# Kernel optimization log

Measured on AMD Instinct MI355X. Metric: run time of the kernel, lower is better.

## Reference

```python
import jax, jax.numpy as jnp
import numpy as np

V, E, H, B, S, T, OOV = 50000, 128, 256, 32, 400, 16, 20


def setup_inputs() -> dict:
    key = jax.random.key(0)
    ks = jax.random.split(key, 20)
    def p(i, shape, s=0.02):
        return jax.random.normal(ks[i], shape, dtype=jnp.float32) * s
    z = lambda *shape: jnp.zeros(shape, dtype=jnp.float32)
    return {
        'input_seq': jax.random.randint(ks[0], (B, S), 0, V),
        'input_seq_ext': jax.random.randint(ks[1], (B, S), 0, V + OOV),
        'target_seq': jax.random.randint(ks[2], (B, T), 0, V),
        'embedding': p(3, (V, E)),
        'enc_Wih_f': p(4, (3 * H, E)), 'enc_Whh_f': p(5, (3 * H, H)),
        'enc_bih_f': z(3 * H), 'enc_bhh_f': z(3 * H),
        'enc_Wih_b': p(6, (3 * H, E)), 'enc_Whh_b': p(7, (3 * H, H)),
        'enc_bih_b': z(3 * H), 'enc_bhh_b': z(3 * H),
        'proj_W': p(8, (H, 2 * H)), 'proj_b': z(H),
        'bridge_W': p(9, (H, 2 * H)), 'bridge_b': z(H),
        'dec_Wih': p(10, (3 * H, E + 2 * H)), 'dec_Whh': p(11, (3 * H, H)),
        'dec_bih': z(3 * H), 'dec_bhh': z(3 * H),
        'attn_Wq': p(12, (H, H)), 'attn_We': p(13, (1, H)),
        'lin_W': p(14, (H, E + 3 * H)), 'lin_b': z(H),
        'pgen_W': p(15, (1, E + 3 * H)), 'pgen_b': z(1),
        'out_W': p(16, (V, H)), 'out_b': z(V),
    }


def gru_cell(x, h, Wih, Whh, bih, bhh):
    # PyTorch GRU cell math
    gi = x @ Wih.T + bih
    gh = h @ Whh.T + bhh
    ir, iz, inn = jnp.split(gi, 3, axis=-1)
    hr, hz, hn = jnp.split(gh, 3, axis=-1)
    r = jax.nn.sigmoid(ir + hr)
    zg = jax.nn.sigmoid(iz + hz)
    n = jnp.tanh(inn + r * hn)
    return (1.0 - zg) * n + zg * h


def run_gru(xs, h0, Wih, Whh, bih, bhh):
    def step(h, x):
        h2 = gru_cell(x, h, Wih, Whh, bih, bhh)
        return h2, h2
    hT, hs = jax.lax.scan(step, h0, xs)
    return hs, hT


def reference(input_seq, input_seq_ext, target_seq, embedding,
              enc_Wih_f, enc_Whh_f, enc_bih_f, enc_bhh_f,
              enc_Wih_b, enc_Whh_b, enc_bih_b, enc_bhh_b,
              proj_W, proj_b, bridge_W, bridge_b,
              dec_Wih, dec_Whh, dec_bih, dec_bhh,
              attn_Wq, attn_We, lin_W, lin_b,
              pgen_W, pgen_b, out_W, out_b):
    Bsz, Slen = input_seq.shape
    Tlen = target_seq.shape[1]
    Hd = bridge_W.shape[0]
    dt = embedding.dtype

    # ---- encoder (bidirectional GRU) ----
    emb_src = embedding[input_seq].transpose(1, 0, 2)  # (S,B,E)
    h0e = jnp.zeros((Bsz, Hd), dt)
    hs_f, hf = run_gru(emb_src, h0e, enc_Wih_f, enc_Whh_f, enc_bih_f, enc_bhh_f)
    hs_b_rev, hb = run_gru(emb_src[::-1], h0e, enc_Wih_b, enc_Whh_b, enc_bih_b, enc_bhh_b)
    enc_states = jnp.concatenate([hs_f, hs_b_rev[::-1]], axis=-1)  # (S,B,2H)
    proj = enc_states @ proj_W.T + proj_b                           # (S,B,H)
    h = jnp.tanh(jnp.concatenate([hf, hb], axis=-1) @ bridge_W.T + bridge_b)  # (B,H)

    rows = jnp.arange(Bsz)
    toks = target_seq[:, :Tlen - 1].T  # teacher forcing, (T-1,B)

    def dec_step(h, tok):
        e = embedding[tok]                                            # (B,E)
        scores = jnp.tanh(h @ attn_Wq.T + proj) @ attn_We[0]          # (S,B)
        alphas = jax.nn.softmax(scores, axis=0)                       # softmax over seq dim
        context = jnp.einsum('sb,sbd->bd', alphas, enc_states)        # (B,2H)
        h2 = gru_cell(jnp.concatenate([e, context], axis=-1), h,
                      dec_Wih, dec_Whh, dec_bih, dec_bhh)             # (B,H)
        cat = jnp.concatenate([e, h2, context], axis=-1)              # (B,E+3H)
        p_gen = jax.nn.sigmoid(cat @ pgen_W.T + pgen_b)               # (B,1)
        logits = (cat @ lin_W.T + lin_b) @ out_W.T + out_b            # (B,V)
        gen = p_gen * jax.nn.softmax(logits, axis=-1)
        attn = (1.0 - p_gen) * alphas.T                               # (B,S)
        ext = jnp.concatenate([gen, jnp.zeros((Bsz, OOV), dt)], axis=-1) + 1e-12
        ext = ext.at[rows[:, None], input_seq_ext].add(attn)          # scatter_add copy dist
        return h2, jnp.log(ext)

    _, outs = jax.lax.scan(dec_step, h, toks)                         # (T-1,B,V+OOV)
    out0 = jnp.zeros((1,) + outs.shape[1:], outs.dtype)               # t=0 row stays zero
    return jnp.concatenate([out0, outs], axis=0)                      # (T,B,V+OOV)
```

## Files before the change

kernel.cpp:

```cpp
#include <hip/hip_runtime.h>

#define SLEN 400
#define BATCH 32
#define TLEN 16
#define NDEC 15
#define EDIM 128
#define HDIM 256
#define H3 768
#define VVOC 50000
#define VEXT 50020
#define SCHUNK 50

__device__ __forceinline__ float frcp(float x){ return __builtin_amdgcn_rcpf(x); }
__device__ __forceinline__ float fsig(float x){ return frcp(1.f + __expf(-x)); }
__device__ __forceinline__ float ftanh(float x){
  float e = __expf(2.f*x);
  return 1.f - 2.f*frcp(e + 1.f);
}

typedef _Float16 h2 __attribute__((ext_vector_type(2)));
typedef _Float16 half8 __attribute__((ext_vector_type(8)));
typedef float floatx4 __attribute__((ext_vector_type(4)));

__device__ __forceinline__ h2 u2h(unsigned u){ return __builtin_bit_cast(h2, u); }
__device__ __forceinline__ unsigned pkh(float a, float b){
  h2 v; v.x=(_Float16)a; v.y=(_Float16)b;
  return __builtin_bit_cast(unsigned, v);
}

#if __has_builtin(__builtin_amdgcn_fdot2)
__device__ __forceinline__ float fdot2h(h2 a, h2 b, float c){
  return __builtin_amdgcn_fdot2(a, b, c, false);
}
#else
__device__ __forceinline__ float fdot2h(h2 a, h2 b, float c){
  return fmaf((float)a.x,(float)b.x, fmaf((float)a.y,(float)b.y, c));
}
#endif

#if __has_builtin(__builtin_amdgcn_sdot4)
__device__ __forceinline__ int sdot4(unsigned a, unsigned b, int c){
  return __builtin_amdgcn_sdot4((int)a, (int)b, c, false);
}
#else
__device__ __forceinline__ int sdot4(unsigned a, unsigned b, int c){
  #pragma unroll
  for (int k=0;k<4;++k)
    c += (int)(char)((a>>(8*k))&0xFF) * (int)(char)((b>>(8*k))&0xFF);
  return c;
}
#endif

__device__ __forceinline__ float wred_sum(float v){
  #pragma unroll
  for (int o=32;o>0;o>>=1) v += __shfl_down(v,o,64);
  return v;
}
__device__ __forceinline__ float wred_max(float v){
  #pragma unroll
  for (int o=32;o>0;o>>=1) v = fmaxf(v, __shfl_down(v,o,64));
  return v;
}
__device__ __forceinline__ float block_sum(float v, float* red){
  v = wred_sum(v);
  int lane = threadIdx.x & 63, wid = threadIdx.x >> 6;
  if (!lane) red[wid] = v;
  __syncthreads();
  if (threadIdx.x == 0){
    float m = red[0];
    int nw = blockDim.x >> 6;
    for (int w=1;w<nw;++w) m += red[w];
    red[0] = m;
  }
  __syncthreads();
  v = red[0];
  __syncthreads();
  return v;
}

__global__ __launch_bounds__(64) void k_embed(
    const int* __restrict__ input_seq, const int* __restrict__ target_seq,
    const float* __restrict__ embedding,
    _Float16* __restrict__ emb16, float* __restrict__ cat_all, _Float16* __restrict__ cat16)
{
  int row = blockIdx.x;
  if (row < SLEN*BATCH) {
    int s = row >> 5, b = row & 31;
    int tok = input_seq[b*SLEN + s];
    float2 v = ((const float2*)(embedding + (size_t)tok*EDIM))[threadIdx.x];
    ((unsigned*)(emb16 + (size_t)row*EDIM))[threadIdx.x] = pkh(v.x, v.y);
  } else {
    int rr = row - SLEN*BATCH;
    int t = rr >> 5, b = rr & 31;
    int tok = target_seq[b*TLEN + t];
    float2 v = ((const float2*)(embedding + (size_t)tok*EDIM))[threadIdx.x];
    ((float2*)(cat_all + (size_t)rr*896))[threadIdx.x] = v;
    ((unsigned*)(cat16 + (size_t)rr*896))[threadIdx.x] = pkh(v.x, v.y);
  }
}

__global__ __launch_bounds__(256) void k_cvtv5(
    const float* __restrict__ S0, _Float16* __restrict__ D0, int n0,
    const float* __restrict__ S1, _Float16* __restrict__ D1, int n1,
    const float* __restrict__ S2, _Float16* __restrict__ D2, int n2,
    const float* __restrict__ S3, _Float16* __restrict__ D3, int n3,
    const float* __restrict__ S4, _Float16* __restrict__ D4, int n4)
{
  const float* S; _Float16* D; int n8;
  switch (blockIdx.y){
    case 0: S=S0; D=D0; n8=n0; break;
    case 1: S=S1; D=D1; n8=n1; break;
    case 2: S=S2; D=D2; n8=n2; break;
    case 3: S=S3; D=D3; n8=n3; break;
    default: S=S4; D=D4; n8=n4; break;
  }
  int i = blockIdx.x*256 + threadIdx.x;
  if (i >= n8) return;
  float4 a = ((const float4*)S)[i*2];
  float4 b = ((const float4*)S)[i*2+1];
  uint4 o;
  o.x = pkh(a.x,a.y); o.y = pkh(a.z,a.w);
  o.z = pkh(b.x,b.y); o.w = pkh(b.z,b.w);
  ((uint4*)D)[i] = o;
}

__global__ __launch_bounds__(256) void k_cvtv(
    const float* __restrict__ S, _Float16* __restrict__ D, int n8)
{
  int i = blockIdx.x*256 + threadIdx.x;
  if (i >= n8) return;
  float4 a = ((const float4*)S)[i*2];
  float4 b = ((const float4*)S)[i*2+1];
  uint4 o;
  o.x = pkh(a.x,a.y); o.y = pkh(a.z,a.w);
  o.z = pkh(b.x,b.y); o.w = pkh(b.z,b.w);
  ((uint4*)D)[i] = o;
}

__global__ __launch_bounds__(64) void k_cvtk3(
    const float* __restrict__ W0, uint4* __restrict__ D0,
    const float* __restrict__ W1, uint4* __restrict__ D1,
    const float* __restrict__ W2, uint4* __restrict__ D2)
{
  const float* W; uint4* D; int ldw, coloff, nrows, nk8;
  switch (blockIdx.y){
    case 0: W=W0; D=D0; ldw=640;  coloff=128; nrows=H3;   nk8=64; break;
    case 1: W=W1; D=D1; ldw=HDIM; coloff=0;   nrows=H3;   nk8=32; break;
    default: W=W2; D=D2; ldw=HDIM; coloff=0;  nrows=HDIM; nk8=32; break;
  }
  int row = blockIdx.x, k8 = threadIdx.x;
  if (row >= nrows || k8 >= nk8) return;
  const float* s = W + (size_t)row*ldw + coloff + k8*8;
  float4 x = *(const float4*)s;
  float4 y = *(const float4*)(s+4);
  uint4 o;
  o.x = pkh(x.x,x.y); o.y = pkh(x.z,x.w);
  o.z = pkh(y.x,y.y); o.w = pkh(y.z,y.w);
  D[(size_t)k8*nrows + row] = o;
}

__global__ __launch_bounds__(64) void k_cvti8(
    const float* __restrict__ Wf, uint4* __restrict__ Df,
    const float* __restrict__ Wb, uint4* __restrict__ Db,
    float* __restrict__ scl)
{
  int row = blockIdx.x, dir = blockIdx.y;
  const float* W = dir ? Wb : Wf;
  uint4* D = dir ? Db : Df;
  int t = threadIdx.x;
  const float* src = W + (size_t)row*HDIM;
  float m = 0.f;
  #pragma unroll
  for (int k=0;k<4;++k) m = fmaxf(m, fabsf(src[t*4+k]));
  m = wred_max(m);
  m = __shfl(m, 0, 64);
  float inv = (m > 0.f) ? 127.f/m : 0.f;
  if (t == 0) scl[dir*H3 + row] = (m > 0.f) ? m/(127.f*127.f) : 0.f;
  if (t < 16){
    unsigned u[4];
    #pragma unroll
    for (int q=0;q<4;++q){
      unsigned uu = 0;
      #pragma unroll
      for (int k=0;k<4;++k){
        int iv = (int)rintf(src[t*16 + q*4 + k]*inv);
        iv = iv > 127 ? 127 : (iv < -127 ? -127 : iv);
        uu |= ((unsigned)(iv & 0xFF)) << (8*k);
      }
      u[q] = uu;
    }
    uint4 o; o.x=u[0]; o.y=u[1]; o.z=u[2]; o.w=u[3];
    D[(size_t)t*H3 + row] = o;
  }
}

__global__ __launch_bounds__(256) void k_gmm(
    const _Float16* __restrict__ A, int lda,
    const _Float16* __restrict__ W, int ldw,
    const float* __restrict__ bias,
    float* __restrict__ C, _Float16* __restrict__ C16, int ldc,
    int M, int N, int K, int rev)
{
  __shared__ __align__(16) _Float16 Al[128*64];
  __shared__ __align__(16) _Float16 Wl[128*64];
  int tid = threadIdx.x;
  int wv = tid >> 6, l = tid & 63;
  int wr = (wv>>1)*64, wc = (wv&1)*64;
  int lr = l & 15, lh = l >> 4;
  int m0 = blockIdx.y*128, n0 = blockIdx.x*128;
  floatx4 acc[4][4];
  #pragma unroll
  for (int i=0;i<4;++i)
    #pragma unroll
    for (int jn=0;jn<4;++jn) acc[i][jn] = (floatx4){0.f,0.f,0.f,0.f};

  for (int kc=0; kc<K; kc+=64){
    #pragma unroll
    for (int i=0;i<4;++i){
      int idx = tid + i*256;
      int row = idx>>3, c = idx&7;
      int m = m0+row;
      uint4 v = {0u,0u,0u,0u};
      if (m < M){
        int am = m;
        if (rev){ int s = m>>5; am = ((SLEN-1-s)<<5)|(m&31); }
        v = *(const uint4*)&A[(size_t)am*lda + kc + c*8];
      }
      *(uint4*)&Al[row*64 + ((c ^ (row&7))<<3)] = v;
    }
    #pragma unroll
    for (int i=0;i<4;++i){
      int idx = tid + i*256;
      int row = idx>>3, c = idx&7;
      int n = n0+row;
      uint4 v = {0u,0u,0u,0u};
      if (n < N) v = *(const uint4*)&W[(size_t)n*ldw + kc + c*8];
      *(uint4*)&Wl[row*64 + ((c ^ (row&7))<<3)] = v;
    }
    __syncthreads();
    #pragma unroll
    for (int ks=0; ks<2; ++ks){
      half8 af0, af1, af2, af3, bf0, bf1, bf2, bf3;
      {
        int c = ks*4 + lh;
        int r0 = wr + 0*16 + lr, r1 = wr + 1*16 + lr, r2 = wr + 2*16 + lr, r3 = wr + 3*16 + lr;
        af0 = *(const half8*)&Al[r0*64 + ((c ^ (r0&7))<<3)];
        af1 = *(const half8*)&Al[r1*64 + ((c ^ (r1&7))<<3)];
        af2 = *(const half8*)&Al[r2*64 + ((c ^ (r2&7))<<3)];
        af3 = *(const half8*)&Al[r3*64 + ((c ^ (r3&7))<<3)];
        int n0l = wc + 0*16 + lr, n1l = wc + 1*16 + lr, n2l = wc + 2*16 + lr, n3l = wc + 3*16 + lr;
        bf0 = *(const half8*)&Wl[n0l*64 + ((c ^ (n0l&7))<<3)];
        bf1 = *(const half8*)&Wl[n1l*64 + ((c ^ (n1l&7))<<3)];
        bf2 = *(const half8*)&Wl[n2l*64 + ((c ^ (n2l&7))<<3)];
        bf3 = *(const half8*)&Wl[n3l*64 + ((c ^ (n3l&7))<<3)];
      }
      half8 afs[4] = {af0, af1, af2, af3};
      half8 bfs[4] = {bf0, bf1, bf2, bf3};
      #pragma unroll
      for (int mi=0;mi<4;++mi)
        #pragma unroll
        for (int ni=0;ni<4;++ni)
          acc[mi][ni] = __builtin_amdgcn_mfma_f32_16x16x32_f16(afs[mi], bfs[ni], acc[mi][ni], 0,0,0);
    }
    __syncthreads();
  }
  #pragma unroll
  for (int mi=0;mi<4;++mi){
    #pragma unroll
    for (int q=0;q<4;++q){
      int m = m0 + wr + mi*16 + lh*4 + q;
      if (m < M){
        #pragma unroll
        for (int ni=0;ni<4;++ni){
          int n = n0 + wc + ni*16 + lr;
          if (n < N){
            float v = acc[mi][ni][q] + bias[n];
            if (C)   C[(size_t)m*ldc + n] = v;
            if (C16) C16[(size_t)m*ldc + n] = (_Float16)v;
          }
        }
      }
    }
  }
}

__global__ __launch_bounds__(768) void k_enc(
    const _Float16* __restrict__ gi16_f, const _Float16* __restrict__ gi16_b,
    const uint4* __restrict__ Wi8_f, const uint4* __restrict__ Wi8_b,
    const float* __restrict__ scl_i8,
    const float* __restrict__ bhh_f, const float* __restrict__ bhh_b,
    _Float16* __restrict__ enc16, float* __restrict__ hfin)
{
  int dir = blockIdx.x >> 5, b = blockIdx.x & 31;
  int jj = threadIdx.x;
  const _Float16* gi = dir ? gi16_b : gi16_f;
  const uint4* Wi8p = (dir ? Wi8_b : Wi8_f) + jj;
  float scl = scl_i8[dir*H3 + jj];
  float bh = (dir ? bhh_b : bhh_f)[jj];

  __shared__ __align__(16) unsigned h8u[HDIM/4];
  __shared__ __align__(16) float st[H3];
  __shared__ uint4 Wlds[9][H3];

  #pragma unroll
  for (int p=0;p<9;++p) Wlds[p][jj] = Wi8p[p*H3];

  if (jj < HDIM/4) h8u[jj] = 0u;
  float hreg = 0.f;
  _Float16* dst = enc16 + (size_t)b*2*HDIM + dir*HDIM + jj;
  __syncthreads();

  for (int s=0;s<SLEN;++s){
    const _Float16* grow = gi + ((size_t)s*BATCH + b)*H3;
    float g1 = 0.f, g2 = 0.f;
    if (jj < 512)  g1 = (float)grow[jj];
    if (jj < HDIM) g2 = (float)grow[2*HDIM + jj];
    int is0=0, is1=0, is2=0, is3=0;
    #pragma unroll
    for (int p=0;p<9;++p){
      uint4 w = Wlds[p][jj];
      uint4 hq = *(const uint4*)&h8u[4*p];
      is0 = sdot4(w.x, hq.x, is0);
      is1 = sdot4(w.y, hq.y, is1);
      is2 = sdot4(w.z, hq.z, is2);
      is3 = sdot4(w.w, hq.w, is3);
    }
    #pragma unroll
    for (int p=9;p<16;++p){
      uint4 w = Wi8p[(size_t)p*H3];
      uint4 hq = *(const uint4*)&h8u[4*p];
      is0 = sdot4(w.x, hq.x, is0);
      is1 = sdot4(w.y, hq.y, is1);
      is2 = sdot4(w.z, hq.z, is2);
      is3 = sdot4(w.w, hq.w, is3);
    }
    float acc = (float)((is0+is1)+(is2+is3))*scl + bh;
    st[jj] = (jj < 512) ? (acc + g1) : acc;
    __syncthreads();
    if (jj < HDIM){
      float rr = fsig(st[jj]);
      float zz = fsig(st[HDIM + jj]);
      float nn = ftanh(g2 + rr*st[2*HDIM + jj]);
      float h2v = nn + zz*(hreg - nn);
      hreg = h2v;
      int srow = dir ? (SLEN-1-s) : s;
      dst[(size_t)srow*BATCH*2*HDIM] = (_Float16)h2v;
      int iv = (int)rintf(h2v*127.f);
      iv = iv > 127 ? 127 : (iv < -127 ? -127 : iv);
      ((char*)h8u)[jj] = (char)iv;
      if (s == SLEN-1) hfin[(size_t)(dir*BATCH + b)*HDIM + jj] = h2v;
    }
    __syncthreads();
  }
}

__global__ __launch_bounds__(256) void k_bridge(
    const float* __restrict__ hfin,
    const float* __restrict__ bridge_W, const float* __restrict__ bridge_b,
    float* __restrict__ h_out)
{
  int b = blockIdx.x, j = threadIdx.x;
  __shared__ float hcat[2*HDIM];
  hcat[j]        = hfin[(size_t)b*HDIM + j];
  hcat[HDIM + j] = hfin[(size_t)(BATCH + b)*HDIM + j];
  __syncthreads();
  const float* w = bridge_W + (size_t)j*2*HDIM;
  float4 a = {0.f,0.f,0.f,0.f};
  #pragma unroll 4
  for (int k=0;k<2*HDIM;k+=4){
    float4 h4 = *(const float4*)&hcat[k];
    float4 w4 = *(const float4*)&w[k];
    a.x=fmaf(h4.x,w4.x,a.x); a.y=fmaf(h4.y,w4.y,a.y);
    a.z=fmaf(h4.z,w4.z,a.z); a.w=fmaf(h4.w,w4.w,a.w);
  }
  h_out[b*HDIM+j] = ftanh((a.x+a.y)+(a.z+a.w) + bridge_b[j]);
}

__global__ __launch_bounds__(256) void k_attnB(
    int t,
    const _Float16* __restrict__ proj16,
    const _Float16* __restrict__ enc16,
    const uint4* __restrict__ Wq16k,
    const float* __restrict__ attn_We,
    const float* __restrict__ hin,
    float* __restrict__ alphas_e,
    float* __restrict__ sum_part,
    float* __restrict__ ctx_part)
{
  int ch = blockIdx.x, b = blockIdx.y;
  int tid = threadIdx.x;
  __shared__ float q_s[HDIM], we_s[HDIM], sc[SCHUNK], red[8];
  __shared__ __align__(16) unsigned hq[HDIM/2];

  we_s[tid] = attn_We[tid];
  if (tid < HDIM/2){
    float2 hv = *(const float2*)&hin[b*HDIM + tid*2];
    hq[tid] = pkh(hv.x, hv.y);
  }
  __syncthreads();
  {
    float a0=0.f,a1=0.f,a2=0.f,a3=0.f;
    #pragma unroll
    for (int k8=0;k8<32;++k8){
      uint4 w = Wq16k[(size_t)k8*HDIM + tid];
      uint4 hp = *(const uint4*)&hq[k8*4];
      a0 = fdot2h(u2h(w.x),u2h(hp.x),a0);
      a1 = fdot2h(u2h(w.y),u2h(hp.y),a1);
      a2 = fdot2h(u2h(w.z),u2h(hp.z),a2);
      a3 = fdot2h(u2h(w.w),u2h(hp.w),a3);
    }
    q_s[tid] = (a0+a1)+(a2+a3);
  }
  __syncthreads();
  {
    int wave = tid >> 6, lane = tid & 63;
    int d0 = lane*4;
    float4 qv = *(const float4*)&q_s[d0];
    float4 wv = *(const float4*)&we_s[d0];
    for (int is = wave; is < SCHUNK; is += 4){
      int s = ch*SCHUNK + is;
      uint2 p = *(const uint2*)&proj16[((size_t)(s*BATCH + b))*HDIM + d0];
      h2 pa = u2h(p.x), pb = u2h(p.y);
      float v = ftanh(qv.x+(float)pa.x)*wv.x + ftanh(qv.y+(float)pa.y)*wv.y
              + ftanh(qv.z+(float)pb.x)*wv.z + ftanh(qv.w+(float)pb.y)*wv.w;
      v = wred_sum(v);
      if (lane == 0){
        float e = __expf(v);
        sc[is] = e;
        alphas_e[((size_t)t*SLEN + s)*BATCH + b] = e;
      }
    }
  }
  __syncthreads();
  {
    float sv = (tid < SCHUNK) ? sc[tid] : 0.f;
    sv = block_sum(sv, red);
    if (tid == 0) sum_part[b*8 + ch] = sv;
  }
  {
    float a0=0.f, a1=0.f;
    for (int is=0; is<SCHUNK; ++is){
      int s = ch*SCHUNK + is;
      unsigned u = *(const unsigned*)&enc16[((size_t)(s*BATCH + b) << 9) + tid*2];
      h2 ev = u2h(u);
      float e = sc[is];
      a0 = fmaf(e, (float)ev.x, a0);
      a1 = fmaf(e, (float)ev.y, a1);
    }
    float2 o; o.x = a0; o.y = a1;
    *(float2*)&ctx_part[(((size_t)b*8 + ch) << 9) + tid*2] = o;
  }
}

__global__ __launch_bounds__(256) void k_gruD(
    int t,
    const float* __restrict__ ctx_part,
    const float* __restrict__ sum_part,
    const float* __restrict__ gie_all,
    const uint4* __restrict__ dWck16,
    const uint4* __restrict__ dWhk16,
    const float* __restrict__ dec_bhh,
    const float* __restrict__ hin,
    float* __restrict__ hout,
    float* __restrict__ cat_all, _Float16* __restrict__ cat16,
    float* __restrict__ sums_all)
{
  int ch = blockIdx.x, b = blockIdx.y;
  int tid = threadIdx.x;
  int jl = tid & 31, slice = tid >> 5;
  __shared__ __align__(16) unsigned cpk[HDIM], hpk[HDIM/2];
  __shared__ float hf[HDIM];
  __shared__ float pc[3][8][32], ph[3][8][32];
  __shared__ float invs;

  if (tid == 0){
    float ssum = 0.f;
    #pragma unroll
    for (int c=0;c<8;++c) ssum += sum_part[b*8 + c];
    float inv = 1.f/ssum;
    invs = inv;
    if (ch == 0) sums_all[t*BATCH + b] = inv;
  }
  if (tid < HDIM/2){
    float2 hv = *(const float2*)&hin[b*HDIM + tid*2];
    hpk[tid] = pkh(hv.x, hv.y);
    hf[tid*2] = hv.x; hf[tid*2+1] = hv.y;
  }
  __syncthreads();
  {
    int d0 = tid*2;
    float c0=0.f, c1=0.f;
    #pragma unroll
    for (int c=0;c<8;++c){
      float2 v = *(const float2*)&ctx_part[(((size_t)b*8 + c) << 9) + d0];
      c0 += v.x; c1 += v.y;
    }
    c0 *= invs; c1 *= invs;
    cpk[tid] = pkh(c0, c1);
    if (ch == 0){
      int r = t*BATCH + b;
      cat_all[(size_t)r*896 + 384 + d0]     = c0;
      cat_all[(size_t)r*896 + 384 + d0 + 1] = c1;
      cat16[(size_t)r*896 + 384 + d0]     = (_Float16)c0;
      cat16[(size_t)r*896 + 384 + d0 + 1] = (_Float16)c1;
    }
  }
  __syncthreads();
  {
    int jb = ch*32 + jl;
    float c0=0.f,c1=0.f,c2=0.f, g0=0.f,g1=0.f,g2=0.f;
    #pragma unroll
    for (int i=0;i<8;++i){
      int k8 = slice*8 + i;
      uint4 hq = *(const uint4*)&cpk[k8*4];
      uint4 w0 = dWck16[(size_t)k8*H3 + jb];
      uint4 w1 = dWck16[(size_t)k8*H3 + 256 + jb];
      uint4 w2 = dWck16[(size_t)k8*H3 + 512 + jb];
      c0 = fdot2h(u2h(w0.x),u2h(hq.x),c0); c0 = fdot2h(u2h(w0.y),u2h(hq.y),c0);
      c0 = fdot2h(u2h(w0.z),u2h(hq.z),c0); c0 = fdot2h(u2h(w0.w),u2h(hq.w),c0);
      c1 = fdot2h(u2h(w1.x),u2h(hq.x),c1); c1 = fdot2h(u2h(w1.y),u2h(hq.y),c1);
      c1 = fdot2h(u2h(w1.z),u2h(hq.z),c1); c1 = fdot2h(u2h(w1.w),u2h(hq.w),c1);
      c2 = fdot2h(u2h(w2.x),u2h(hq.x),c2); c2 = fdot2h(u2h(w2.y),u2h(hq.y),c2);
      c2 = fdot2h(u2h(w2.z),u2h(hq.z),c2); c2 = fdot2h(u2h(w2.w),u2h(hq.w),c2);
    }
    #pragma unroll
    for (int i=0;i<4;++i){
      int k8 = slice*4 + i;
      uint4 hq = *(const uint4*)&hpk[k8*4];
      uint4 w0 = dWhk16[(size_t)k8*H3 + jb];
      uint4 w1 = dWhk16[(size_t)k8*H3 + 256 + jb];
      uint4 w2 = dWhk16[(size_t)k8*H3 + 512 + jb];
      g0 = fdot2h(u2h(w0.x),u2h(hq.x),g0); g0 = fdot2h(u2h(w0.y),u2h(hq.y),g0);
      g0 = fdot2h(u2h(w0.z),u2h(hq.z),g0); g0 = fdot2h(u2h(w0.w),u2h(hq.w),g0);
      g1 = fdot2h(u2h(w1.x),u2h(hq.x),g1); g1 = fdot2h(u2h(w1.y),u2h(hq.y),g1);
      g1 = fdot2h(u2h(w1.z),u2h(hq.z),g1); g1 = fdot2h(u2h(w1.w),u2h(hq.w),g1);
      g2 = fdot2h(u2h(w2.x),u2h(hq.x),g2); g2 = fdot2h(u2h(w2.y),u2h(hq.y),g2);
      g2 = fdot2h(u2h(w2.z),u2h(hq.z),g2); g2 = fdot2h(u2h(w2.w),u2h(hq.w),g2);
    }
    pc[0][slice][jl]=c0; pc[1][slice][jl]=c1; pc[2][slice][jl]=c2;
    ph[0][slice][jl]=g0; ph[1][slice][jl]=g1; ph[2][slice][jl]=g2;
  }
  __syncthreads();
  if (tid < 32){
    int j = tid, r = t*BATCH + b;
    int jj = ch*32 + j;
    float gi0 = gie_all[(size_t)r*H3 + jj];
    float gi1 = gie_all[(size_t)r*H3 + 256 + jj];
    float gi2 = gie_all[(size_t)r*H3 + 512 + jj];
    float gh0 = dec_bhh[jj], gh1 = dec_bhh[256 + jj], gh2 = dec_bhh[512 + jj];
    #pragma unroll
    for (int c=0;c<8;++c){
      gi0 += pc[0][c][j]; gi1 += pc[1][c][j]; gi2 += pc[2][c][j];
      gh0 += ph[0][c][j]; gh1 += ph[1][c][j]; gh2 += ph[2][c][j];
    }
    float rr = fsig(gi0 + gh0);
    float zz = fsig(gi1 + gh1);
    float nn = ftanh(gi2 + rr*gh2);
    float hp = hf[jj];
    float h2v = nn + zz*(hp - nn);
    hout[b*HDIM + jj] = h2v;
    cat_all[(size_t)r*896 + 128 + jj] = h2v;
    cat16[(size_t)r*896 + 128 + jj] = (_Float16)h2v;
  }
}

__global__ __launch_bounds__(64) void k_pgen(
    const float* __restrict__ cat_all,
    const float* __restrict__ pgen_W, const float* __restrict__ pgen_b,
    float* __restrict__ pgen_all)
{
  int r = blockIdx.x;
  const float* c = cat_all + (size_t)r*896;
  float acc = 0.f;
  for (int k=threadIdx.x; k<896; k+=64) acc = fmaf(c[k], pgen_W[k], acc);
  acc = wred_sum(acc);
  if (threadIdx.x==0) pgen_all[r] = fsig(acc + pgen_b[0]);
}

__global__ __launch_bounds__(256) void k_rowsum(
    const _Float16* __restrict__ logits, float* __restrict__ row_sum)
{
  int r = blockIdx.x;
  const uint4* row = (const uint4*)(logits + (size_t)r*VVOC);
  __shared__ float red[8];
  float s = 0.f;
  for (int v=threadIdx.x; v<VVOC/8; v+=256){
    uint4 x = row[v];
    h2 a=u2h(x.x), bb=u2h(x.y), c=u2h(x.z), d=u2h(x.w);
    s += __expf((float)a.x) + __expf((float)a.y) + __expf((float)bb.x) + __expf((float)bb.y)
       + __expf((float)c.x) + __expf((float)c.y) + __expf((float)d.x) + __expf((float)d.y);
  }
  s = block_sum(s, red);
  if (threadIdx.x==0) row_sum[r] = 1.f/s;
}

__global__ __launch_bounds__(512) void k_scatter(
    const int* __restrict__ input_seq_ext,
    const float* __restrict__ alphas_e, const float* __restrict__ sums_all,
    const float* __restrict__ pgen_all,
    float* __restrict__ out)
{
  int r = blockIdx.x;
  int s = threadIdx.x;
  if (s >= SLEN) return;
  int t = r >> 5, b = r & 31;
  float w = (1.f - pgen_all[r]) * alphas_e[((size_t)t*SLEN + s)*BATCH + b] * sums_all[r];
  int idx = input_seq_ext[b*SLEN + s];
  atomicAdd(&out[((size_t)(t+1)*BATCH + b)*VEXT + idx], w);
}

__global__ __launch_bounds__(256) void k_final2(
    const _Float16* __restrict__ logits, const float* __restrict__ pgen_all,
    const float* __restrict__ row_sum,
    float* __restrict__ out)
{
  int v = blockIdx.x*256 + threadIdx.x;
  if (v >= VEXT) return;
  int b = blockIdx.y, t = blockIdx.z + 1;
  size_t o = ((size_t)t*BATCH + b)*VEXT + v;
  int r = (t-1)*BATCH + b;
  float val = out[o] + 1e-12f;
  if (v < VVOC)
    val += pgen_all[r] * row_sum[r] * __expf((float)logits[(size_t)r*VVOC + v]);
  out[o] = __logf(val);
}

extern "C" void kernel_launch(void* const* d_in, const int* in_sizes, int n_in,
                              void* d_out, int out_size, void* d_ws, size_t ws_size,
                              hipStream_t stream)
{
  (void)in_sizes; (void)n_in; (void)ws_size;
  const int*   input_seq     = (const int*)d_in[0];
  const int*   input_seq_ext = (const int*)d_in[1];
  const int*   target_seq    = (const int*)d_in[2];
  const float* embedding     = (const float*)d_in[3];
  const float* enc_Wih_f     = (const float*)d_in[4];
  const float* enc_Whh_f     = (const float*)d_in[5];
  const float* enc_bih_f     = (const float*)d_in[6];
  const float* enc_bhh_f     = (const float*)d_in[7];
  const float* enc_Wih_b     = (const float*)d_in[8];
  const float* enc_Whh_b     = (const float*)d_in[9];
  const float* enc_bih_b     = (const float*)d_in[10];
  const float* enc_bhh_b     = (const float*)d_in[11];
  const float* proj_W        = (const float*)d_in[12];
  const float* proj_b        = (const float*)d_in[13];
  const float* bridge_W      = (const float*)d_in[14];
  const float* bridge_b      = (const float*)d_in[15];
  const float* dec_Wih       = (const float*)d_in[16];
  const float* dec_Whh       = (const float*)d_in[17];
  const float* dec_bih       = (const float*)d_in[18];
  const float* dec_bhh       = (const float*)d_in[19];
  const float* attn_Wq       = (const float*)d_in[20];
  const float* attn_We       = (const float*)d_in[21];
  const float* lin_W         = (const float*)d_in[22];
  const float* lin_b         = (const float*)d_in[23];
  const float* pgen_W        = (const float*)d_in[24];
  const float* pgen_b        = (const float*)d_in[25];
  const float* out_W         = (const float*)d_in[26];
  const float* out_b         = (const float*)d_in[27];
  float* out = (float*)d_out;
  float* ws  = (float*)d_ws;

  _Float16* emb16    = (_Float16*)(ws + 0);
  _Float16* Wih16_f  = (_Float16*)(ws + 409600);
  _Float16* Wih16_b  = (_Float16*)(ws + 458752);
  _Float16* proj_W16 = (_Float16*)(ws + 507904);
  _Float16* lin_W16  = (_Float16*)(ws + 573440);
  _Float16* cat16    = (_Float16*)(ws + 688128);
  _Float16* lin16    = (_Float16*)(ws + 903168);
  _Float16* dWih16   = (_Float16*)(ws + 964608);
  _Float16* enc16    = (_Float16*)(ws + 1638400);
  float* hfin        = ws + 4915200;
  _Float16* proj16   = (_Float16*)(ws + 8192000);
  _Float16* gi16_f   = (_Float16*)(ws + 11468800);
  _Float16* gi16_b   = (_Float16*)(ws + 16384000);
  _Float16* logits16 = (_Float16*)(ws + 11468800);
  _Float16* out_W16  = (_Float16*)(ws + 23468800);
  uint4* Wq16k       = (uint4*)(ws + 33145600);
  uint4* dWck16      = (uint4*)(ws + 33178368);
  uint4* dWhk16      = (uint4*)(ws + 33374976);
  float* ctx_part    = ws + 33473280;
  float* sum_part    = ws + 33604352;
  float* sums_all    = ws + 33604608;
  float* hbuf0       = ws + 33605088;
  float* hbuf1       = ws + 33613280;
  uint4* Wi8_f       = (uint4*)(ws + 33621472);
  uint4* Wi8_b       = (uint4*)(ws + 33670624);
  float* scl_i8      = ws + 33719776;
  float* cat_all     = ws + 35468800;
  float* gie_all     = ws + 35898880;
  float* alphas_e    = ws + 36275712;
  float* pgen_all    = ws + 36467712;
  float* row_sum     = ws + 36468192;

  (void)hipMemsetAsync(out, 0, (size_t)out_size*sizeof(float), stream);

  k_embed<<<dim3(SLEN*BATCH + NDEC*BATCH), dim3(64), 0, stream>>>(
      input_seq, target_seq, embedding, emb16, cat_all, cat16);

  k_cvtv5<<<dim3(240, 5), dim3(256), 0, stream>>>(
      enc_Wih_f, Wih16_f, 12288,
      enc_Wih_b, Wih16_b, 12288,
      proj_W,    proj_W16, 16384,
      lin_W,     lin_W16,  28672,
      dec_Wih,   dWih16,   61440);
  k_cvtk3<<<dim3(H3, 3), dim3(64), 0, stream>>>(
      dec_Wih,   dWck16,
      dec_Whh,   dWhk16,
      attn_Wq,   Wq16k);
  k_cvti8<<<dim3(H3, 2), dim3(64), 0, stream>>>(enc_Whh_f, Wi8_f, enc_Whh_b, Wi8_b, scl_i8);

  k_gmm<<<dim3(6,100), dim3(256), 0, stream>>>(emb16, EDIM, Wih16_f, EDIM, enc_bih_f,
      (float*)nullptr, gi16_f, H3, SLEN*BATCH, H3, EDIM, 0);
  k_gmm<<<dim3(6,100), dim3(256), 0, stream>>>(emb16, EDIM, Wih16_b, EDIM, enc_bih_b,
      (float*)nullptr, gi16_b, H3, SLEN*BATCH, H3, EDIM, 1);

  k_enc<<<dim3(64), dim3(768), 0, stream>>>(gi16_f, gi16_b, Wi8_f, Wi8_b,
      scl_i8, enc_bhh_f, enc_bhh_b, enc16, hfin);

  k_cvtv<<<dim3((12800000/8+255)/256), dim3(256), 0, stream>>>(out_W, out_W16, 12800000/8);

  k_gmm<<<dim3(2,100), dim3(256), 0, stream>>>(enc16, 2*HDIM, proj_W16, 2*HDIM, proj_b,
      (float*)nullptr, proj16, HDIM, SLEN*BATCH, HDIM, 2*HDIM, 0);

  k_bridge<<<dim3(BATCH), dim3(256), 0, stream>>>(hfin, bridge_W, bridge_b, hbuf0);

  k_gmm<<<dim3(6,4), dim3(256), 0, stream>>>(cat16, 896, dWih16, 640, dec_bih,
      gie_all, (_Float16*)nullptr, H3, NDEC*BATCH, H3, EDIM, 0);

  float* hb[2] = {hbuf0, hbuf1};
  for (int t=0;t<NDEC;++t){
    k_attnB<<<dim3(8,32), dim3(256), 0, stream>>>(t, proj16, enc16, Wq16k, attn_We,
        hb[t&1], alphas_e, sum_part, ctx_part);
    k_gruD<<<dim3(8,32), dim3(256), 0, stream>>>(t, ctx_part, sum_part, gie_all,
        dWck16, dWhk16, dec_bhh, hb[t&1], hb[(t+1)&1], cat_all, cat16, sums_all);
  }

  k_gmm<<<dim3(2,4), dim3(256), 0, stream>>>(cat16, 896, lin_W16, 896, lin_b,
      (float*)nullptr, lin16, HDIM, NDEC*BATCH, HDIM, 896, 0);
  k_pgen<<<dim3(NDEC*BATCH), dim3(64), 0, stream>>>(cat_all, pgen_W, pgen_b, pgen_all);
  k_gmm<<<dim3(391,4), dim3(256), 0, stream>>>(lin16, HDIM, out_W16, HDIM, out_b,
      (float*)nullptr, logits16, VVOC, NDEC*BATCH, VVOC, HDIM, 0);
  k_rowsum<<<dim3(NDEC*BATCH), dim3(256), 0, stream>>>(logits16, row_sum);
  k_scatter<<<dim3(NDEC*BATCH), dim3(512), 0, stream>>>(input_seq_ext, alphas_e, sums_all, pgen_all, out);
  k_final2<<<dim3(196, BATCH, NDEC), dim3(256), 0, stream>>>(logits16, pgen_all, row_sum, out);
}
```

Measured before the change: 1.022 ms.

## Fuse out_W conversion into encoder, softmax rowsum into GEMM, query proj into GRU

The out_W fp32-to-fp16 conversion now runs in 200 extra blocks of the encoder recurrence kernel, so it overlaps with the latency-bound serial encoder instead of being a separate launch. The softmax exp-sum moves into the vocab GEMM epilogue through shuffle reduction and atomics, which removes the k_rowsum pass over the logits. The attention query projection is computed as per-chunk partials in the decoder GRU kernel (and in the bridge for the first step), so k_attnB only sums those partials. The encoder LDS weight cache also drops from 9 to 8 slices. The costs are atomic contention, exp sums taken from fp32 values rather than fp16-rounded ones, and possible slowdown of the encoder from the co-resident conversion blocks.

After: 1.136 ms. 1.11x slower.

```diff
diff --git a/kernel.cpp b/kernel.cpp
--- a/kernel.cpp
+++ b/kernel.cpp
@@ -124,19 +124,6 @@
   ((uint4*)D)[i] = o;
 }
 
-__global__ __launch_bounds__(256) void k_cvtv(
-    const float* __restrict__ S, _Float16* __restrict__ D, int n8)
-{
-  int i = blockIdx.x*256 + threadIdx.x;
-  if (i >= n8) return;
-  float4 a = ((const float4*)S)[i*2];
-  float4 b = ((const float4*)S)[i*2+1];
-  uint4 o;
-  o.x = pkh(a.x,a.y); o.y = pkh(a.z,a.w);
-  o.z = pkh(b.x,b.y); o.w = pkh(b.z,b.w);
-  ((uint4*)D)[i] = o;
-}
-
 __global__ __launch_bounds__(64) void k_cvtk3(
     const float* __restrict__ W0, uint4* __restrict__ D0,
     const float* __restrict__ W1, uint4* __restrict__ D1,
@@ -199,7 +186,7 @@
     const _Float16* __restrict__ W, int ldw,
     const float* __restrict__ bias,
     float* __restrict__ C, _Float16* __restrict__ C16, int ldc,
-    int M, int N, int K, int rev)
+    int M, int N, int K, int rev, float* __restrict__ expsum)
 {
   __shared__ __align__(16) _Float16 Al[128*64];
   __shared__ __align__(16) _Float16 Wl[128*64];
@@ -269,6 +256,7 @@
     #pragma unroll
     for (int q=0;q<4;++q){
       int m = m0 + wr + mi*16 + lh*4 + q;
+      float psum = 0.f;
       if (m < M){
         #pragma unroll
         for (int ni=0;ni<4;++ni){
@@ -277,8 +265,14 @@
             float v = acc[mi][ni][q] + bias[n];
             if (C)   C[(size_t)m*ldc + n] = v;
             if (C16) C16[(size_t)m*ldc + n] = (_Float16)v;
+            if (expsum) psum += __expf(v);
           }
         }
+      }
+      if (expsum){
+        #pragma unroll
+        for (int o=8;o>0;o>>=1) psum += __shfl_down(psum, o, 16);
+        if (lr == 0 && m < M) atomicAdd(&expsum[m], psum);
       }
     }
   }
@@ -289,8 +283,22 @@
     const uint4* __restrict__ Wi8_f, const uint4* __restrict__ Wi8_b,
     const float* __restrict__ scl_i8,
     const float* __restrict__ bhh_f, const float* __restrict__ bhh_b,
-    _Float16* __restrict__ enc16, float* __restrict__ hfin)
-{
+    _Float16* __restrict__ enc16, float* __restrict__ hfin,
+    const float* __restrict__ outW, _Float16* __restrict__ outW16)
+{
+  if (blockIdx.x >= 64){
+    int idx = (int)(blockIdx.x - 64)*768 + (int)threadIdx.x;
+    const int stride = 200*768;
+    for (int i = idx; i < 1600000; i += stride){
+      float4 a = ((const float4*)outW)[i*2];
+      float4 b2 = ((const float4*)outW)[i*2+1];
+      uint4 o;
+      o.x = pkh(a.x,a.y); o.y = pkh(a.z,a.w);
+      o.z = pkh(b2.x,b2.y); o.w = pkh(b2.z,b2.w);
+      ((uint4*)outW16)[i] = o;
+    }
+    return;
+  }
   int dir = blockIdx.x >> 5, b = blockIdx.x & 31;
   int jj = threadIdx.x;
   const _Float16* gi = dir ? gi16_b : gi16_f;
@@ -300,10 +308,10 @@
 
   __shared__ __align__(16) unsigned h8u[HDIM/4];
   __shared__ __align__(16) float st[H3];
-  __shared__ uint4 Wlds[9][H3];
-
-  #pragma unroll
-  for (int p=0;p<9;++p) Wlds[p][jj] = Wi8p[p*H3];
+  __shared__ uint4 Wlds[8][H3];
+
+  #pragma unroll
+  for (int p=0;p<8;++p) Wlds[p][jj] = Wi8p[p*H3];
 
   if (jj < HDIM/4) h8u[jj] = 0u;
   float hreg = 0.f;
@@ -317,7 +325,7 @@
     if (jj < HDIM) g2 = (float)grow[2*HDIM + jj];
     int is0=0, is1=0, is2=0, is3=0;
     #pragma unroll
-    for (int p=0;p<9;++p){
+    for (int p=0;p<8;++p){
       uint4 w = Wlds[p][jj];
       uint4 hq = *(const uint4*)&h8u[4*p];
       is0 = sdot4(w.x, hq.x, is0);
@@ -326,7 +334,7 @@
       is3 = sdot4(w.w, hq.w, is3);
     }
     #pragma unroll
-    for (int p=9;p<16;++p){
+    for (int p=8;p<16;++p){
       uint4 w = Wi8p[(size_t)p*H3];
       uint4 hq = *(const uint4*)&h8u[4*p];
       is0 = sdot4(w.x, hq.x, is0);
@@ -357,10 +365,12 @@
 __global__ __launch_bounds__(256) void k_bridge(
     const float* __restrict__ hfin,
     const float* __restrict__ bridge_W, const float* __restrict__ bridge_b,
-    float* __restrict__ h_out)
+    const uint4* __restrict__ Wq16k,
+    float* __restrict__ h_out, float* __restrict__ q_part)
 {
   int b = blockIdx.x, j = threadIdx.x;
   __shared__ float hcat[2*HDIM];
+  __shared__ float h0s[HDIM];
   hcat[j]        = hfin[(size_t)b*HDIM + j];
   hcat[HDIM + j] = hfin[(size_t)(BATCH + b)*HDIM + j];
   __syncthreads();
@@ -373,16 +383,32 @@
     a.x=fmaf(h4.x,w4.x,a.x); a.y=fmaf(h4.y,w4.y,a.y);
     a.z=fmaf(h4.z,w4.z,a.z); a.w=fmaf(h4.w,w4.w,a.w);
   }
-  h_out[b*HDIM+j] = ftanh((a.x+a.y)+(a.z+a.w) + bridge_b[j]);
+  float h0 = ftanh((a.x+a.y)+(a.z+a.w) + bridge_b[j]);
+  h_out[b*HDIM+j] = h0;
+  h0s[j] = h0;
+  __syncthreads();
+  float qp = 0.f;
+  #pragma unroll
+  for (int k8=0;k8<32;++k8){
+    uint4 wq = Wq16k[(size_t)k8*HDIM + j];
+    const float* hb8 = &h0s[k8*8];
+    h2 w0=u2h(wq.x), w1=u2h(wq.y), w2=u2h(wq.z), w3=u2h(wq.w);
+    qp = fmaf((float)w0.x, hb8[0], qp); qp = fmaf((float)w0.y, hb8[1], qp);
+    qp = fmaf((float)w1.x, hb8[2], qp); qp = fmaf((float)w1.y, hb8[3], qp);
+    qp = fmaf((float)w2.x, hb8[4], qp); qp = fmaf((float)w2.y, hb8[5], qp);
+    qp = fmaf((float)w3.x, hb8[6], qp); qp = fmaf((float)w3.y, hb8[7], qp);
+  }
+  q_part[((size_t)b*8 + 0)*HDIM + j] = qp;
+  #pragma unroll
+  for (int c=1;c<8;++c) q_part[((size_t)b*8 + c)*HDIM + j] = 0.f;
 }
 
 __global__ __launch_bounds__(256) void k_attnB(
     int t,
     const _Float16* __restrict__ proj16,
     const _Float16* __restrict__ enc16,
-    const uint4* __restrict__ Wq16k,
+    const float* __restrict__ q_part,
     const float* __restrict__ attn_We,
-    const float* __restrict__ hin,
     float* __restrict__ alphas_e,
     float* __restrict__ sum_part,
     float* __restrict__ ctx_part)
@@ -390,26 +416,13 @@
   int ch = blockIdx.x, b = blockIdx.y;
   int tid = threadIdx.x;
   __shared__ float q_s[HDIM], we_s[HDIM], sc[SCHUNK], red[8];
-  __shared__ __align__(16) unsigned hq[HDIM/2];
 
   we_s[tid] = attn_We[tid];
-  if (tid < HDIM/2){
-    float2 hv = *(const float2*)&hin[b*HDIM + tid*2];
-    hq[tid] = pkh(hv.x, hv.y);
-  }
-  __syncthreads();
   {
-    float a0=0.f,a1=0.f,a2=0.f,a3=0.f;
-    #pragma unroll
-    for (int k8=0;k8<32;++k8){
-      uint4 w = Wq16k[(size_t)k8*HDIM + tid];
-      uint4 hp = *(const uint4*)&hq[k8*4];
-      a0 = fdot2h(u2h(w.x),u2h(hp.x),a0);
-      a1 = fdot2h(u2h(w.y),u2h(hp.y),a1);
-      a2 = fdot2h(u2h(w.z),u2h(hp.z),a2);
-      a3 = fdot2h(u2h(w.w),u2h(hp.w),a3);
-    }
-    q_s[tid] = (a0+a1)+(a2+a3);
+    float q = 0.f;
+    #pragma unroll
+    for (int c=0;c<8;++c) q += q_part[((size_t)b*8 + c)*HDIM + tid];
+    q_s[tid] = q;
   }
   __syncthreads();
   {
@@ -459,11 +472,12 @@
     const float* __restrict__ gie_all,
     const uint4* __restrict__ dWck16,
     const uint4* __restrict__ dWhk16,
+    const uint4* __restrict__ Wq16k,
     const float* __restrict__ dec_bhh,
     const float* __restrict__ hin,
     float* __restrict__ hout,
     float* __restrict__ cat_all, _Float16* __restrict__ cat16,
-    float* __restrict__ sums_all)
+    float* __restrict__ sums_all, float* __restrict__ q_part)
 {
   int ch = blockIdx.x, b = blockIdx.y;
   int tid = threadIdx.x;
@@ -471,6 +485,7 @@
   __shared__ __align__(16) unsigned cpk[HDIM], hpk[HDIM/2];
   __shared__ float hf[HDIM];
   __shared__ float pc[3][8][32], ph[3][8][32];
+  __shared__ float hch[32];
   __shared__ float invs;
 
   if (tid == 0){
@@ -561,6 +576,22 @@
     hout[b*HDIM + jj] = h2v;
     cat_all[(size_t)r*896 + 128 + jj] = h2v;
     cat16[(size_t)r*896 + 128 + jj] = (_Float16)h2v;
+    hch[j] = h2v;
+  }
+  __syncthreads();
+  {
+    float qp = 0.f;
+    #pragma unroll
+    for (int kk=0; kk<4; ++kk){
+      uint4 wq = Wq16k[(size_t)(ch*4+kk)*HDIM + tid];
+      const float* hb8 = &hch[kk*8];
+      h2 w0=u2h(wq.x), w1=u2h(wq.y), w2=u2h(wq.z), w3=u2h(wq.w);
+      qp = fmaf((float)w0.x, hb8[0], qp); qp = fmaf((float)w0.y, hb8[1], qp);
+      qp = fmaf((float)w1.x, hb8[2], qp); qp = fmaf((float)w1.y, hb8[3], qp);
+      qp = fmaf((float)w2.x, hb8[4], qp); qp = fmaf((float)w2.y, hb8[5], qp);
+      qp = fmaf((float)w3.x, hb8[6], qp); qp = fmaf((float)w3.y, hb8[7], qp);
+    }
+    q_part[((size_t)b*8 + ch)*HDIM + tid] = qp;
   }
 }
 
@@ -575,23 +606,6 @@
   for (int k=threadIdx.x; k<896; k+=64) acc = fmaf(c[k], pgen_W[k], acc);
   acc = wred_sum(acc);
   if (threadIdx.x==0) pgen_all[r] = fsig(acc + pgen_b[0]);
-}
-
-__global__ __launch_bounds__(256) void k_rowsum(
-    const _Float16* __restrict__ logits, float* __restrict__ row_sum)
-{
-  int r = blockIdx.x;
-  const uint4* row = (const uint4*)(logits + (size_t)r*VVOC);
-  __shared__ float red[8];
-  float s = 0.f;
-  for (int v=threadIdx.x; v<VVOC/8; v+=256){
-    uint4 x = row[v];
-    h2 a=u2h(x.x), bb=u2h(x.y), c=u2h(x.z), d=u2h(x.w);
-    s += __expf((float)a.x) + __expf((float)a.y) + __expf((float)bb.x) + __expf((float)bb.y)
-       + __expf((float)c.x) + __expf((float)c.y) + __expf((float)d.x) + __expf((float)d.y);
-  }
-  s = block_sum(s, red);
-  if (threadIdx.x==0) row_sum[r] = 1.f/s;
 }
 
 __global__ __launch_bounds__(512) void k_scatter(
@@ -621,7 +635,7 @@
   int r = (t-1)*BATCH + b;
   float val = out[o] + 1e-12f;
   if (v < VVOC)
-    val += pgen_all[r] * row_sum[r] * __expf((float)logits[(size_t)r*VVOC + v]);
+    val += pgen_all[r] * frcp(row_sum[r]) * __expf((float)logits[(size_t)r*VVOC + v]);
   out[o] = __logf(val);
 }
 
@@ -687,6 +701,7 @@
   uint4* Wi8_f       = (uint4*)(ws + 33621472);
   uint4* Wi8_b       = (uint4*)(ws + 33670624);
   float* scl_i8      = ws + 33719776;
+  float* q_part      = ws + 33721312;
   float* cat_all     = ws + 35468800;
   float* gie_all     = ws + 35898880;
   float* alphas_e    = ws + 36275712;
@@ -694,6 +709,7 @@
   float* row_sum     = ws + 36468192;
 
   (void)hipMemsetAsync(out, 0, (size_t)out_size*sizeof(float), stream);
+  (void)hipMemsetAsync(row_sum, 0, 480*sizeof(float), stream);
 
   k_embed<<<dim3(SLEN*BATCH + NDEC*BATCH), dim3(64), 0, stream>>>(
       input_seq, target_seq, embedding, emb16, cat_all, cat16);
@@ -711,37 +727,36 @@
   k_cvti8<<<dim3(H3, 2), dim3(64), 0, stream>>>(enc_Whh_f, Wi8_f, enc_Whh_b, Wi8_b, scl_i8);
 
   k_gmm<<<dim3(6,100), dim3(256), 0, stream>>>(emb16, EDIM, Wih16_f, EDIM, enc_bih_f,
-      (float*)nullptr, gi16_f, H3, SLEN*BATCH, H3, EDIM, 0);
+      (float*)nullptr, gi16_f, H3, SLEN*BATCH, H3, EDIM, 0, (float*)nullptr);
   k_gmm<<<dim3(6,100), dim3(256), 0, stream>>>(emb16, EDIM, Wih16_b, EDIM, enc_bih_b,
-      (float*)nullptr, gi16_b, H3, SLEN*BATCH, H3, EDIM, 1);
-
-  k_enc<<<dim3(64), dim3(768), 0, stream>>>(gi16_f, gi16_b, Wi8_f, Wi8_b,
-      scl_i8, enc_bhh_f, enc_bhh_b, enc16, hfin);
-
-  k_cvtv<<<dim3((12800000/8+255)/256), dim3(256), 0, stream>>>(out_W, out_W16, 12800000/8);
+      (float*)nullptr, gi16_b, H3, SLEN*BATCH, H3, EDIM, 1, (float*)nullptr);
+
+  k_enc<<<dim3(264), dim3(768), 0, stream>>>(gi16_f, gi16_b, Wi8_f, Wi8_b,
+      scl_i8, enc_bhh_f, enc_bhh_b, enc16, hfin, out_W, out_W16);
 
   k_gmm<<<dim3(2,100), dim3(256), 0, stream>>>(enc16, 2*HDIM, proj_W16, 2*HDIM, proj_b,
-      (float*)nullptr, proj16, HDIM, SLEN*BATCH, HDIM, 2*HDIM, 0);
-
-  k_bridge<<<dim3(BATCH), dim3(256), 0, stream>>>(hfin, bridge_W, bridge_b, hbuf0);
+      (float*)nullptr, proj16, HDIM, SLEN*BATCH, HDIM, 2*HDIM, 0, (float*)nullptr);
+
+  k_bridge<<<dim3(BATCH), dim3(256), 0, stream>>>(hfin, bridge_W, bridge_b, Wq16k,
+      hbuf0, q_part);
 
   k_gmm<<<dim3(6,4), dim3(256), 0, stream>>>(cat16, 896, dWih16, 640, dec_bih,
-      gie_all, (_Float16*)nullptr, H3, NDEC*BATCH, H3, EDIM, 0);
+      gie_all, (_Float16*)nullptr, H3, NDEC*BATCH, H3, EDIM, 0, (float*)nullptr);
 
   float* hb[2] = {hbuf0, hbuf1};
   for (int t=0;t<NDEC;++t){
-    k_attnB<<<dim3(8,32), dim3(256), 0, stream>>>(t, proj16, enc16, Wq16k, attn_We,
-        hb[t&1], alphas_e, sum_part, ctx_part);
+    k_attnB<<<dim3(8,32), dim3(256), 0, stream>>>(t, proj16, enc16, q_part, attn_We,
+        alphas_e, sum_part, ctx_part);
     k_gruD<<<dim3(8,32), dim3(256), 0, stream>>>(t, ctx_part, sum_part, gie_all,
-        dWck16, dWhk16, dec_bhh, hb[t&1], hb[(t+1)&1], cat_all, cat16, sums_all);
+        dWck16, dWhk16, Wq16k, dec_bhh, hb[t&1], hb[(t+1)&1], cat_all, cat16,
+        sums_all, q_part);
   }
 
   k_gmm<<<dim3(2,4), dim3(256), 0, stream>>>(cat16, 896, lin_W16, 896, lin_b,
-      (float*)nullptr, lin16, HDIM, NDEC*BATCH, HDIM, 896, 0);
+      (float*)nullptr, lin16, HDIM, NDEC*BATCH, HDIM, 896, 0, (float*)nullptr);
   k_pgen<<<dim3(NDEC*BATCH), dim3(64), 0, stream>>>(cat_all, pgen_W, pgen_b, pgen_all);
   k_gmm<<<dim3(391,4), dim3(256), 0, stream>>>(lin16, HDIM, out_W16, HDIM, out_b,
-      (float*)nullptr, logits16, VVOC, NDEC*BATCH, VVOC, HDIM, 0);
-  k_rowsum<<<dim3(NDEC*BATCH), dim3(256), 0, stream>>>(logits16, row_sum);
+      (float*)nullptr, logits16, VVOC, NDEC*BATCH, VVOC, HDIM, 0, row_sum);
   k_scatter<<<dim3(NDEC*BATCH), dim3(512), 0, stream>>>(input_seq_ext, alphas_e, sums_all, pgen_all, out);
   k_final2<<<dim3(196, BATCH, NDEC), dim3(256), 0, stream>>>(logits16, pgen_all, row_sum, out);
 }
```
